# Kernel optimization log

Measured on AMD Instinct MI355X. Metric: run time of the kernel, lower is better.

Reference implementation:

```python
import jax, jax.numpy as jnp
import numpy as np

T = 2048
HID = 4096
H = 32
HKV = 8
D = 128
EPS = 1e-5
THETA = 1e6
WINDOW = 1024


def setup_inputs() -> dict:
    key = jax.random.key(0)
    k1, k2, k3 = jax.random.split(key, 3)
    return {
        "positions": jnp.arange(T, dtype=jnp.int32),
        "hidden_states": jax.random.normal(k1, (T, HID), dtype=jnp.float32),
        "w_qkv": jax.random.normal(k2, (HID, (H + 2 * HKV) * D), dtype=jnp.float32) * 0.02,
        "q_norm_w": jnp.ones((D,), dtype=jnp.float32),
        "k_norm_w": jnp.ones((D,), dtype=jnp.float32),
        "w_o": jax.random.normal(k3, (H * D, HID), dtype=jnp.float32) * 0.02,
    }


def _rmsnorm(x, w):
    # per-head RMSNorm over last dim (head_dim)
    var = jnp.mean(x * x, axis=-1, keepdims=True)
    return x * jax.lax.rsqrt(var + EPS) * w


def _rope_neox(x, positions):
    # x: [T, heads, D]; neox style: rotate halves
    half = D // 2
    inv_freq = 1.0 / (THETA ** (jnp.arange(0, half, dtype=jnp.float32) / half))
    ang = positions.astype(jnp.float32)[:, None] * inv_freq  # [T, half]
    cos = jnp.cos(ang)[:, None, :]
    sin = jnp.sin(ang)[:, None, :]
    x1, x2 = x[..., :half], x[..., half:]
    return jnp.concatenate([x1 * cos - x2 * sin, x2 * cos + x1 * sin], axis=-1)


def reference(positions, hidden_states, w_qkv, q_norm_w, k_norm_w, w_o):
    qkv = hidden_states @ w_qkv  # [T, (H+2Hkv)*D]
    q, k, v = jnp.split(qkv, [H * D, (H + HKV) * D], axis=-1)
    q = _rmsnorm(q.reshape(T, H, D), q_norm_w)
    k = _rmsnorm(k.reshape(T, HKV, D), k_norm_w)
    v = v.reshape(T, HKV, D)

    q = _rope_neox(q, positions)
    k = _rope_neox(k, positions)

    # GQA: expand kv heads to H
    rep = H // HKV
    k = jnp.repeat(k, rep, axis=1)  # [T, H, D]
    v = jnp.repeat(v, rep, axis=1)

    scale = D ** -0.5
    scores = jnp.einsum('thd,shd->hts', q, k) * scale  # [H, T, T]
    i = jnp.arange(T)[:, None]
    j = jnp.arange(T)[None, :]
    mask = (j <= i) & (i - j < WINDOW)  # causal + sliding window
    scores = jnp.where(mask[None], scores, -jnp.inf)
    probs = jax.nn.softmax(scores, axis=-1)
    attn = jnp.einsum('hts,shd->thd', probs, v).reshape(T, H * D)
    return attn @ w_o
```

## Files before the change

### kernel.cpp

```cpp
#include <hip/hip_runtime.h>
#include <hip/hip_bf16.h>
#include <stdint.h>

#define T_SEQ  2048
#define HIDDEN 4096
#define NHEAD  32
#define NKV    8
#define HDIM   128
#define NQKV   6144
#define WINDOW 1024
#define SCALE  0.08838834764831845f
#define SHIFT  12.0f

typedef __attribute__((ext_vector_type(8))) short          short8;
typedef __attribute__((ext_vector_type(8))) unsigned short ushort8_t;
typedef __attribute__((ext_vector_type(4))) float          floatx4;

__device__ __forceinline__ unsigned short f2bf(float f) {
    union { float f; unsigned int u; } v; v.f = f;
    unsigned int u = v.u;
    unsigned int r = (u + 0x7FFFu + ((u >> 16) & 1u)) >> 16;
    return (unsigned short)r;
}
__device__ __forceinline__ float bf2f(unsigned short u) {
    union { unsigned int u; float f; } v; v.u = ((unsigned int)u) << 16;
    return v.f;
}

#define GLOBAL_AS(p) ((const __attribute__((address_space(1))) void*)(p))
#define LDS_AS(p)    ((__attribute__((address_space(3))) void*)(p))

#define S_BARRIER() do { asm volatile("" ::: "memory");  \
                         __builtin_amdgcn_s_barrier();   \
                         asm volatile("" ::: "memory"); } while (0)

__global__ __launch_bounds__(256) void convert_bf16_kernel(
        const float* __restrict__ X, unsigned short* __restrict__ Y, int n4) {
    int i = blockIdx.x * blockDim.x + threadIdx.x;
    if (i < n4) {
        float4 v = ((const float4*)X)[i];
        ushort4 o;
        o.x = f2bf(v.x); o.y = f2bf(v.y); o.z = f2bf(v.z); o.w = f2bf(v.w);
        ((ushort4*)Y)[i] = o;
    }
}

__global__ __launch_bounds__(256) void transpose_bf16_kernel(
        const float* __restrict__ W, unsigned short* __restrict__ Wt, int K, int N) {
    __shared__ float tile[128][33];
    const int n0 = blockIdx.x * 32, k0 = blockIdx.y * 128;
    const int tid = threadIdx.x;
    const int rr = tid >> 3, cc = tid & 7;
    #pragma unroll
    for (int p = 0; p < 4; ++p) {
        int r = p * 32 + rr;
        float4 v = *(const float4*)&W[(size_t)(k0 + r) * N + n0 + cc * 4];
        tile[r][cc * 4 + 0] = v.x; tile[r][cc * 4 + 1] = v.y;
        tile[r][cc * 4 + 2] = v.z; tile[r][cc * 4 + 3] = v.w;
    }
    __syncthreads();
    const int nL = tid >> 3, kc = tid & 7;
    #pragma unroll
    for (int q = 0; q < 2; ++q) {
        int kbase = kc * 8 + q * 64;
        ushort8_t o;
        #pragma unroll
        for (int j = 0; j < 8; ++j) o[j] = f2bf(tile[kbase + j][nL]);
        *(ushort8_t*)&Wt[(size_t)(n0 + nL) * K + k0 + kbase] = o;
    }
}

#define STG3_A(bufi, kt, r)                                                       \
    __builtin_amdgcn_global_load_lds(                                             \
        GLOBAL_AS(A + (size_t)(m0 + rRow[r]) * K + ((kt) << 6) + rOff[r]),        \
        LDS_AS(&As3[bufi][((r) * 256 + tid) * 8]), 16, 0, 0)
#define STG3_B(bufi, kt, r)                                                       \
    __builtin_amdgcn_global_load_lds(                                             \
        GLOBAL_AS(B + (size_t)(n0 + rRow[r]) * K + ((kt) << 6) + rOff[r]),        \
        LDS_AS(&Bs3[bufi][((r) * 256 + tid) * 8]), 16, 0, 0)

template <bool BF16_OUT>
__global__ __launch_bounds__(256, 2) void gemm_bt3_kernel(
        const unsigned short* __restrict__ A,
        const unsigned short* __restrict__ B,
        void* __restrict__ Cv, int M, int N, int K) {
    __shared__ __align__(16) unsigned short As3[2][128 * 64];
    __shared__ __align__(16) unsigned short Bs3[2][128 * 64];

    const int tid  = threadIdx.x;
    const int lane = tid & 63, wave = tid >> 6;
    const int wr = wave >> 1, wc = wave & 1;
    const int lrow = lane & 15, hi = lane >> 4;

    const int nwg = gridDim.x * gridDim.y;
    int wg = blockIdx.y * gridDim.x + blockIdx.x;
    wg = (wg & 7) * (nwg >> 3) + (wg >> 3);
    const int bx = wg % gridDim.x;
    const int by = wg / gridDim.x;
    const int m0 = by * 128, n0 = bx * 128;

    const int NT = K >> 6;

    int rRow[4], rOff[4];
    #pragma unroll
    for (int r = 0; r < 4; ++r) {
        int idx = r * 256 + tid;
        int row = idx >> 3;
        rRow[r] = row;
        rOff[r] = ((idx & 7) ^ (row & 7)) * 8;
    }

    const int sA0   = (hi ^ (lrow & 7)) * 8;
    const int aBase = (wr * 64 + lrow) * 64;
    const int bBase = (wc * 64 + lrow) * 64;

    floatx4 acc[4][4] = {};

    auto compute_tile = [&](int cur) {
        const unsigned short* ap = &As3[cur][0];
        const unsigned short* bp = &Bs3[cur][0];
        short8 af[4][2], bf[4][2];
        #pragma unroll
        for (int m = 0; m < 4; ++m)
            #pragma unroll
            for (int kh = 0; kh < 2; ++kh)
                af[m][kh] = *(const short8*)(ap + aBase + m * 1024 + (sA0 ^ (kh << 5)));
        #pragma unroll
        for (int n = 0; n < 4; ++n)
            #pragma unroll
            for (int kh = 0; kh < 2; ++kh)
                bf[n][kh] = *(const short8*)(bp + bBase + n * 1024 + (sA0 ^ (kh << 5)));
        __builtin_amdgcn_s_setprio(1);
        #pragma unroll
        for (int m = 0; m < 4; ++m)
            #pragma unroll
            for (int n = 0; n < 4; ++n) {
                acc[m][n] = __builtin_amdgcn_mfma_f32_16x16x32_bf16(
                    af[m][0], bf[n][0], acc[m][n], 0, 0, 0);
                acc[m][n] = __builtin_amdgcn_mfma_f32_16x16x32_bf16(
                    af[m][1], bf[n][1], acc[m][n], 0, 0, 0);
            }
        __builtin_amdgcn_s_setprio(0);
    };

    #pragma unroll
    for (int r = 0; r < 4; ++r) STG3_A(0, 0, r);
    #pragma unroll
    for (int r = 0; r < 4; ++r) STG3_B(0, 0, r);
    asm volatile("s_waitcnt vmcnt(0)" ::: "memory");
    S_BARRIER();

    for (int t = 0; t < NT - 1; ++t) {
        const int cur = t & 1;
        #pragma unroll
        for (int r = 0; r < 4; ++r) STG3_A(cur ^ 1, t + 1, r);
        #pragma unroll
        for (int r = 0; r < 4; ++r) STG3_B(cur ^ 1, t + 1, r);
        compute_tile(cur);
        asm volatile("s_waitcnt vmcnt(0)" ::: "memory");
        S_BARRIER();
    }
    compute_tile((NT - 1) & 1);

    const int rowb = hi * 4, col = lrow;
    #pragma unroll
    for (int mi = 0; mi < 4; ++mi)
        #pragma unroll
        for (int ni = 0; ni < 4; ++ni) {
            size_t base = (size_t)(m0 + wr * 64 + mi * 16 + rowb) * N
                        + (n0 + wc * 64 + ni * 16 + col);
            #pragma unroll
            for (int r = 0; r < 4; ++r) {
                if (BF16_OUT)
                    ((unsigned short*)Cv)[base + (size_t)r * N] = f2bf(acc[mi][ni][r]);
                else
                    ((float*)Cv)[base + (size_t)r * N] = acc[mi][ni][r];
            }
        }
}

#define STG4_A(bufi, kt, r)                                                       \
    __builtin_amdgcn_global_load_lds(                                             \
        GLOBAL_AS(A + (size_t)(m0 + rRowA[r]) * K + ((kt) << 6) + rOffA[r]),      \
        LDS_AS(&As4[bufi][((r) * 256 + tid) * 8]), 16, 0, 0)
#define STG4_B(bufi, kt, r)                                                       \
    __builtin_amdgcn_global_load_lds(                                             \
        GLOBAL_AS(B + (size_t)(n0 + rRowB[r]) * K + ((kt) << 6) + rOffB[r]),      \
        LDS_AS(&Bs4[bufi][((r) * 256 + tid) * 8]), 16, 0, 0)

template <bool BF16_OUT>
__global__ __launch_bounds__(256, 2) void gemm_bt4_kernel(
        const unsigned short* __restrict__ A,
        const unsigned short* __restrict__ B,
        void* __restrict__ Cv, int M, int N, int K) {
    __shared__ __align__(16) unsigned short As4[2][128 * 64];
    __shared__ __align__(16) unsigned short Bs4[2][192 * 64];

    const int tid  = threadIdx.x;
    const int lane = tid & 63, wave = tid >> 6;
    const int wr = wave >> 1, wc = wave & 1;
    const int lrow = lane & 15, hi = lane >> 4;

    const int nwg = gridDim.x * gridDim.y;
    int wg = blockIdx.y * gridDim.x + blockIdx.x;
    wg = (wg & 7) * (nwg >> 3) + (wg >> 3);
    const int by = wg % gridDim.x;
    const int bx = wg / gridDim.x;
    const int m0 = by * 128, n0 = bx * 192;

    const int NT = K >> 6;

    int rRowA[4], rOffA[4];
    #pragma unroll
    for (int r = 0; r < 4; ++r) {
        int idx = r * 256 + tid;
        int row = idx >> 3;
        rRowA[r] = row;
        rOffA[r] = ((idx & 7) ^ (row & 7)) * 8;
    }
    int rRowB[6], rOffB[6];
    #pragma unroll
    for (int r = 0; r < 6; ++r) {
        int idx = r * 256 + tid;
        int row = idx >> 3;
        rRowB[r] = row;
        rOffB[r] = ((idx & 7) ^ (row & 7)) * 8;
    }

    const int sA0   = (hi ^ (lrow & 7)) * 8;
    const int aBase = (wr * 64 + lrow) * 64;
    const int bBase = (wc * 96 + lrow) * 64;

    floatx4 acc[4][6] = {};

    auto compute_tile = [&](int cur) {
        const unsigned short* ap = &As4[cur][0];
        const unsigned short* bp = &Bs4[cur][0];
        short8 af[4][2], bf[6][2];
        #pragma unroll
        for (int m = 0; m < 4; ++m)
            #pragma unroll
            for (int kh = 0; kh < 2; ++kh)
                af[m][kh] = *(const short8*)(ap + aBase + m * 1024 + (sA0 ^ (kh << 5)));
        #pragma unroll
        for (int n = 0; n < 6; ++n)
            #pragma unroll
            for (int kh = 0; kh < 2; ++kh)
                bf[n][kh] = *(const short8*)(bp + bBase + n * 1024 + (sA0 ^ (kh << 5)));
        __builtin_amdgcn_s_setprio(1);
        #pragma unroll
        for (int m = 0; m < 4; ++m)
            #pragma unroll
            for (int n = 0; n < 6; ++n) {
                acc[m][n] = __builtin_amdgcn_mfma_f32_16x16x32_bf16(
                    af[m][0], bf[n][0], acc[m][n], 0, 0, 0);
                acc[m][n] = __builtin_amdgcn_mfma_f32_16x16x32_bf16(
                    af[m][1], bf[n][1], acc[m][n], 0, 0, 0);
            }
        __builtin_amdgcn_s_setprio(0);
    };

    #pragma unroll
    for (int r = 0; r < 4; ++r) STG4_A(0, 0, r);
    #pragma unroll
    for (int r = 0; r < 6; ++r) STG4_B(0, 0, r);
    asm volatile("s_waitcnt vmcnt(0)" ::: "memory");
    S_BARRIER();

    for (int t = 0; t < NT - 1; ++t) {
        const int cur = t & 1;
        #pragma unroll
        for (int r = 0; r < 4; ++r) STG4_A(cur ^ 1, t + 1, r);
        #pragma unroll
        for (int r = 0; r < 6; ++r) STG4_B(cur ^ 1, t + 1, r);
        compute_tile(cur);
        asm volatile("s_waitcnt vmcnt(0)" ::: "memory");
        S_BARRIER();
    }
    compute_tile((NT - 1) & 1);

    const int rowb = hi * 4, col = lrow;
    #pragma unroll
    for (int mi = 0; mi < 4; ++mi)
        #pragma unroll
        for (int ni = 0; ni < 6; ++ni) {
            size_t base = (size_t)(m0 + wr * 64 + mi * 16 + rowb) * N
                        + (n0 + wc * 96 + ni * 16 + col);
            #pragma unroll
            for (int r = 0; r < 4; ++r) {
                if (BF16_OUT)
                    ((unsigned short*)Cv)[base + (size_t)r * N] = f2bf(acc[mi][ni][r]);
                else
                    ((float*)Cv)[base + (size_t)r * N] = acc[mi][ni][r];
            }
        }
}

__global__ __launch_bounds__(256) void rope_table_kernel(
        const int* __restrict__ positions, float2* __restrict__ rope) {
    int idx = blockIdx.x * 256 + threadIdx.x;
    int t = idx >> 6, i = idx & 63;
    float inv_freq = expf((float)i * -0.2158673524681918f);
    float sn, cs;
    sincosf((float)positions[t] * inv_freq, &sn, &cs);
    rope[idx] = make_float2(cs, sn);
}

__global__ __launch_bounds__(256) void qkv_post_kernel(
        const unsigned short* __restrict__ qkv, const float2* __restrict__ rope,
        const float* __restrict__ qw, const float* __restrict__ kw,
        unsigned short* __restrict__ qb,
        unsigned short* __restrict__ kb,
        unsigned short* __restrict__ vbT) {
    const int head = blockIdx.y;
    const int t0   = blockIdx.x * 32;
    const int tid  = threadIdx.x;

    if (head < 40) {
        const int r  = tid >> 3;
        const int q8 = tid & 7;
        const int t  = t0 + r;
        const unsigned short* src = qkv + (size_t)t * NQKV
                         + (head < 32 ? head * 128 : 4096 + (head - 32) * 128)
                         + q8 * 16;
        const float* w = (head < 32) ? qw : kw;

        ushort8_t u0 = *(const ushort8_t*)src;
        ushort8_t u1 = *(const ushort8_t*)(src + 8);
        float x[16];
        #pragma unroll
        for (int j = 0; j < 8; ++j) { x[j] = bf2f(u0[j]); x[8 + j] = bf2f(u1[j]); }

        float ss = 0.f;
        #pragma unroll
        for (int j = 0; j < 16; ++j) ss = fmaf(x[j], x[j], ss);
        ss += __shfl_xor(ss, 1); ss += __shfl_xor(ss, 2); ss += __shfl_xor(ss, 4);
        float sc = rsqrtf(ss * (1.f / 128.f) + 1e-5f);

        float xn[16], xp[16];
        #pragma unroll
        for (int j = 0; j < 16; ++j) xn[j] = x[j] * sc * w[q8 * 16 + j];
        #pragma unroll
        for (int j = 0; j < 16; ++j) xp[j] = __shfl_xor(xn[j], 4);

        const float2* rp = rope + (size_t)t * 64 + (q8 & 3) * 16;
        ushort8_t o0, o1;
        #pragma unroll
        for (int j = 0; j < 8; ++j) {
            float2 cs = rp[j];
            float res = (q8 < 4) ? (xn[j] * cs.x - xp[j] * cs.y)
                                 : (xn[j] * cs.x + xp[j] * cs.y);
            o0[j] = f2bf(res);
        }
        #pragma unroll
        for (int j = 0; j < 8; ++j) {
            float2 cs = rp[8 + j];
            float res = (q8 < 4) ? (xn[8+j] * cs.x - xp[8+j] * cs.y)
                                 : (xn[8+j] * cs.x + xp[8+j] * cs.y);
            o1[j] = f2bf(res);
        }
        unsigned short* dst = (head < 32)
            ? qb + ((size_t)t * 32 + head) * 128 + q8 * 16
            : kb + ((size_t)t * 8 + (head - 32)) * 128 + q8 * 16;
        *(ushort8_t*)dst       = o0;
        *(ushort8_t*)(dst + 8) = o1;
    } else {
        __shared__ float tile[128][33];
        const int hk = head - 40;
        {
            const int r = tid >> 3, c8 = tid & 7;
            const unsigned short* src =
                qkv + (size_t)(t0 + r) * NQKV + 5120 + hk * 128 + c8 * 16;
            ushort8_t u0 = *(const ushort8_t*)src;
            ushort8_t u1 = *(const ushort8_t*)(src + 8);
            #pragma unroll
            for (int j = 0; j < 8; ++j) {
                tile[c8 * 16 + j][r]     = bf2f(u0[j]);
                tile[c8 * 16 + 8 + j][r] = bf2f(u1[j]);
            }
        }
        __syncthreads();
        {
            const int d = tid >> 1, th = tid & 1;
            ushort8_t o0, o1;
            #pragma unroll
            for (int j = 0; j < 8; ++j) o0[j] = f2bf(tile[d][th * 16 + j]);
            #pragma unroll
            for (int j = 0; j < 8; ++j) o1[j] = f2bf(tile[d][th * 16 + 8 + j]);
            unsigned short* dst = vbT + ((size_t)hk * 128 + d) * T_SEQ + t0 + th * 16;
            *(ushort8_t*)dst       = o0;
            *(ushort8_t*)(dst + 8) = o1;
        }
    }
}

__global__ __launch_bounds__(256) void attention_kernel(
        const unsigned short* __restrict__ qb,
        const unsigned short* __restrict__ kb,
        const unsigned short* __restrict__ vbT,
        unsigned short* __restrict__ attnb) {
    const int h    = blockIdx.x & 31;
    const int Q0   = (blockIdx.x >> 5) * 64;
    const int tid  = threadIdx.x, wave = tid >> 6, lane = tid & 63;
    const int keyA = lane & 15, g = lane >> 4;
    const int hk   = h >> 2;
    const int qlo  = Q0 + wave * 16;

    __shared__ __align__(16) unsigned short ks [32 * 128];
    __shared__ __align__(16) unsigned short vsT[128 * 32];
    __shared__ __align__(16) unsigned short Pa [4 * 16 * 40];

    unsigned short* pw = Pa + wave * 640;

    short8 qa[4];
    {
        const unsigned short* qp = qb + ((size_t)(qlo + keyA) * 32 + h) * 128 + g * 8;
        #pragma unroll
        for (int s = 0; s < 4; ++s) qa[s] = *(const short8*)(qp + s * 32);
    }

    floatx4 acc[8] = {};
    float l_part[4] = {0.f, 0.f, 0.f, 0.f};

    const int s_begin = (Q0 >= WINDOW) ? ((Q0 - (WINDOW - 1)) & ~31) : 0;
    const int s_end   = Q0 + 63;

    for (int s0 = s_begin; s0 <= s_end; s0 += 32) {
        #pragma unroll
        for (int i = 0; i < 2; ++i) {
            int c = i * 256 + tid;
            {   int row = c >> 4, u = c & 15, su = u ^ (row & 7);
                const unsigned short* kp = kb + ((size_t)(s0 + row) * 8 + hk) * 128 + su * 8;
                __builtin_amdgcn_global_load_lds(GLOBAL_AS(kp), LDS_AS(ks + c * 8), 16, 0, 0); }
            {   int d = c >> 2, u = c & 3, su = u ^ (d & 3);
                const unsigned short* vp = vbT + ((size_t)hk * 128 + d) * T_SEQ + s0 + su * 8;
                __builtin_amdgcn_global_load_lds(GLOBAL_AS(vp), LDS_AS(vsT + c * 8), 16, 0, 0); }
        }
        __syncthreads();

        if (s0 <= qlo + 15 && s0 + 31 >= qlo - (WINDOW - 1)) {
            floatx4 sa0 = {}, sa1 = {};
            #pragma unroll
            for (int kst = 0; kst < 4; ++kst) {
                int u = g + 4 * kst;
                short8 k0 = *(const short8*)(ks + keyA * 128 + (u ^ (keyA & 7)) * 8);
                short8 k1 = *(const short8*)(ks + (16 + keyA) * 128 + (u ^ ((16 + keyA) & 7)) * 8);
                sa0 = __builtin_amdgcn_mfma_f32_16x16x32_bf16(qa[kst], k0, sa0, 0, 0, 0);
                sa1 = __builtin_amdgcn_mfma_f32_16x16x32_bf16(qa[kst], k1, sa1, 0, 0, 0);
            }
            float p0[4], p1[4];
            #pragma unroll
            for (int r = 0; r < 4; ++r) {
                int row = qlo + 4 * g + r;
                int sA = s0 + keyA, sB = sA + 16;
                bool vA = (sA <= row) && (row - sA < WINDOW);
                bool vB = (sB <= row) && (row - sB < WINDOW);
                p0[r] = vA ? __expf(fmaf(sa0[r], SCALE, -SHIFT)) : 0.f;
                p1[r] = vB ? __expf(fmaf(sa1[r], SCALE, -SHIFT)) : 0.f;
                l_part[r] += p0[r] + p1[r];
            }
            #pragma unroll
            for (int r = 0; r < 4; ++r) {
                pw[(4 * g + r) * 40 + keyA]      = f2bf(p0[r]);
                pw[(4 * g + r) * 40 + keyA + 16] = f2bf(p1[r]);
            }
            short8 pf = *(const short8*)(pw + keyA * 40 + g * 8);

            #pragma unroll
            for (int t = 0; t < 8; ++t) {
                int d = t * 16 + keyA;
                short8 vf = *(const short8*)(vsT + d * 32 + (g ^ (d & 3)) * 8);
                acc[t] = __builtin_amdgcn_mfma_f32_16x16x32_bf16(pf, vf, acc[t], 0, 0, 0);
            }
        }
        __syncthreads();
    }

    float inv[4];
    #pragma unroll
    for (int r = 0; r < 4; ++r) {
        float l = l_part[r];
        l += __shfl_xor(l, 1); l += __shfl_xor(l, 2);
        l += __shfl_xor(l, 4); l += __shfl_xor(l, 8);
        inv[r] = 1.f / l;
    }
    #pragma unroll
    for (int t = 0; t < 8; ++t)
        #pragma unroll
        for (int r = 0; r < 4; ++r)
            attnb[(size_t)(qlo + 4 * g + r) * 4096 + h * 128 + t * 16 + keyA] =
                f2bf(acc[t][r] * inv[r]);
}

extern "C" void kernel_launch(void* const* d_in, const int* in_sizes, int n_in,
                              void* d_out, int out_size, void* d_ws, size_t ws_size,
                              hipStream_t stream) {
    const int*   positions = (const int*)  d_in[0];
    const float* hs        = (const float*)d_in[1];
    const float* w_qkv     = (const float*)d_in[2];
    const float* q_norm_w  = (const float*)d_in[3];
    const float* k_norm_w  = (const float*)d_in[4];
    const float* w_o       = (const float*)d_in[5];
    float* out = (float*)d_out;

    char* ws = (char*)d_ws;
    unsigned short* hsb   = (unsigned short*)(ws);
    unsigned short* wqkvt = (unsigned short*)(ws + (size_t)(16u << 20));
    unsigned short* wot   = (unsigned short*)(ws + (size_t)(64u << 20));
    unsigned short* qkvb  = (unsigned short*)(ws + (size_t)(96u << 20));
    unsigned short* qb    = (unsigned short*)(ws + (size_t)(16u << 20));
    unsigned short* kb    = (unsigned short*)(ws + (size_t)(32u << 20));
    unsigned short* vbT   = (unsigned short*)(ws + (size_t)(36u << 20));
    float2*         rope  = (float2*)        (ws + (size_t)(40u << 20));
    unsigned short* attnb = hsb;

    convert_bf16_kernel<<<dim3((T_SEQ * HIDDEN / 4 + 255) / 256), 256, 0, stream>>>(
        hs, hsb, T_SEQ * HIDDEN / 4);
    transpose_bf16_kernel<<<dim3(NQKV / 32, HIDDEN / 128), 256, 0, stream>>>(
        w_qkv, wqkvt, HIDDEN, NQKV);
    transpose_bf16_kernel<<<dim3(HIDDEN / 32, HIDDEN / 128), 256, 0, stream>>>(
        w_o, wot, HIDDEN, HIDDEN);
    gemm_bt4_kernel<true><<<dim3(T_SEQ / 128, NQKV / 192), 256, 0, stream>>>(
        hsb, wqkvt, qkvb, T_SEQ, NQKV, HIDDEN);
    rope_table_kernel<<<dim3(T_SEQ * 64 / 256), 256, 0, stream>>>(positions, rope);
    qkv_post_kernel<<<dim3(T_SEQ / 32, 48), 256, 0, stream>>>(
        qkvb, rope, q_norm_w, k_norm_w, qb, kb, vbT);
    attention_kernel<<<dim3((T_SEQ / 64) * NHEAD), 256, 0, stream>>>(
        qb, kb, vbT, attnb);
    gemm_bt3_kernel<false><<<dim3(HIDDEN / 128, T_SEQ / 128), 256, 0, stream>>>(
        attnb, wot, out, T_SEQ, HIDDEN, HIDDEN);
}
```

Measured before the change: 504.2 us.

## Double-buffer K/V tiles in attention kernel to overlap loads with MFMA

Splits the K and V shared-memory tiles into two buffers and issues the global-to-LDS loads for the next key block before computing on the current one. Only one wait-and-barrier per iteration remains, and it now happens after compute. The goal is to hide global load latency behind the QK and PV MFMA work. LDS use for K/V doubles, which may reduce occupancy.

New measurement: 505.6 us. No clear change (+0.3%).

```diff
diff --git a/kernel.cpp b/kernel.cpp
--- a/kernel.cpp
+++ b/kernel.cpp
@@ -406,11 +406,36 @@
     const int hk   = h >> 2;
     const int qlo  = Q0 + wave * 16;
 
-    __shared__ __align__(16) unsigned short ks [32 * 128];
-    __shared__ __align__(16) unsigned short vsT[128 * 32];
+    __shared__ __align__(16) unsigned short ks [2][32 * 128];
+    __shared__ __align__(16) unsigned short vsT[2][128 * 32];
     __shared__ __align__(16) unsigned short Pa [4 * 16 * 40];
 
     unsigned short* pw = Pa + wave * 640;
+
+    int kRow[2], kOff[2], vD[2], vOff[2];
+    #pragma unroll
+    for (int i = 0; i < 2; ++i) {
+        int c = i * 256 + tid;
+        {   int row = c >> 4, u = c & 15;
+            kRow[i] = row; kOff[i] = (u ^ (row & 7)) * 8; }
+        {   int d = c >> 2, u = c & 3;
+            vD[i] = d; vOff[i] = (u ^ (d & 3)) * 8; }
+    }
+
+    auto stage = [&](int buf, int s0) {
+        #pragma unroll
+        for (int i = 0; i < 2; ++i) {
+            int c = i * 256 + tid;
+            const unsigned short* kp =
+                kb + ((size_t)(s0 + kRow[i]) * 8 + hk) * 128 + kOff[i];
+            __builtin_amdgcn_global_load_lds(GLOBAL_AS(kp),
+                LDS_AS(&ks[buf][c * 8]), 16, 0, 0);
+            const unsigned short* vp =
+                vbT + ((size_t)hk * 128 + vD[i]) * T_SEQ + s0 + vOff[i];
+            __builtin_amdgcn_global_load_lds(GLOBAL_AS(vp),
+                LDS_AS(&vsT[buf][c * 8]), 16, 0, 0);
+        }
+    };
 
     short8 qa[4];
     {
@@ -425,26 +450,23 @@
     const int s_begin = (Q0 >= WINDOW) ? ((Q0 - (WINDOW - 1)) & ~31) : 0;
     const int s_end   = Q0 + 63;
 
+    stage(0, s_begin);
+    asm volatile("s_waitcnt vmcnt(0)" ::: "memory");
+    S_BARRIER();
+
+    int cur = 0;
     for (int s0 = s_begin; s0 <= s_end; s0 += 32) {
-        #pragma unroll
-        for (int i = 0; i < 2; ++i) {
-            int c = i * 256 + tid;
-            {   int row = c >> 4, u = c & 15, su = u ^ (row & 7);
-                const unsigned short* kp = kb + ((size_t)(s0 + row) * 8 + hk) * 128 + su * 8;
-                __builtin_amdgcn_global_load_lds(GLOBAL_AS(kp), LDS_AS(ks + c * 8), 16, 0, 0); }
-            {   int d = c >> 2, u = c & 3, su = u ^ (d & 3);
-                const unsigned short* vp = vbT + ((size_t)hk * 128 + d) * T_SEQ + s0 + su * 8;
-                __builtin_amdgcn_global_load_lds(GLOBAL_AS(vp), LDS_AS(vsT + c * 8), 16, 0, 0); }
-        }
-        __syncthreads();
+        if (s0 + 32 <= s_end) stage(cur ^ 1, s0 + 32);
 
         if (s0 <= qlo + 15 && s0 + 31 >= qlo - (WINDOW - 1)) {
+            const unsigned short* ksb  = &ks[cur][0];
+            const unsigned short* vsb  = &vsT[cur][0];
             floatx4 sa0 = {}, sa1 = {};
             #pragma unroll
             for (int kst = 0; kst < 4; ++kst) {
                 int u = g + 4 * kst;
-                short8 k0 = *(const short8*)(ks + keyA * 128 + (u ^ (keyA & 7)) * 8);
-                short8 k1 = *(const short8*)(ks + (16 + keyA) * 128 + (u ^ ((16 + keyA) & 7)) * 8);
+                short8 k0 = *(const short8*)(ksb + keyA * 128 + (u ^ (keyA & 7)) * 8);
+                short8 k1 = *(const short8*)(ksb + (16 + keyA) * 128 + (u ^ ((16 + keyA) & 7)) * 8);
                 sa0 = __builtin_amdgcn_mfma_f32_16x16x32_bf16(qa[kst], k0, sa0, 0, 0, 0);
                 sa1 = __builtin_amdgcn_mfma_f32_16x16x32_bf16(qa[kst], k1, sa1, 0, 0, 0);
             }
@@ -469,11 +491,13 @@
             #pragma unroll
             for (int t = 0; t < 8; ++t) {
                 int d = t * 16 + keyA;
-                short8 vf = *(const short8*)(vsT + d * 32 + (g ^ (d & 3)) * 8);
+                short8 vf = *(const short8*)(vsb + d * 32 + (g ^ (d & 3)) * 8);
                 acc[t] = __builtin_amdgcn_mfma_f32_16x16x32_bf16(pf, vf, acc[t], 0, 0, 0);
             }
         }
-        __syncthreads();
+        asm volatile("s_waitcnt vmcnt(0)" ::: "memory");
+        S_BARRIER();
+        cur ^= 1;
     }
 
     float inv[4];
```
